# Kernel tuning notes

Hardware: AMD Instinct MI355X
Metric: run time of the kernel (lower is better)

The kernel has to match this reference:

```python
import jax, jax.numpy as jnp
import numpy as np

LN_EPS = 1e-5

def setup_inputs() -> dict:
    key = jax.random.key(0)
    k1, k2, k3 = jax.random.split(key, 3)
    L, B, D = 2048, 8, 1024
    x = jax.random.normal(k1, (L, B, D), dtype=jnp.float32)
    c = jnp.zeros((B, D), dtype=jnp.float32)
    W = jax.random.normal(k2, (D, 3 * D), dtype=jnp.float32) * 0.02
    # bias init from _init_bias: u-bias 0, f-bias 0.5, r-bias 0
    b = jnp.concatenate([jnp.zeros(D), jnp.full((D,), 0.5), jnp.zeros(D)]).astype(jnp.float32)
    gamma = jnp.ones((D,), dtype=jnp.float32)
    beta = jnp.zeros((D,), dtype=jnp.float32)
    return {"x": x, "c": c, "W": W, "b": b, "gamma": gamma, "beta": beta}

def reference(x, c, W, b, gamma, beta):
    # LayerNorm over last dim
    mu = jnp.mean(x, axis=-1, keepdims=True)
    var = jnp.mean(jnp.square(x - mu), axis=-1, keepdims=True)
    x_norm = (x - mu) * jax.lax.rsqrt(var + LN_EPS) * gamma + beta
    # Fused u/f/r projection: [L,B,3D]
    ufr = jnp.einsum('lbd,de->lbe', x_norm, W) + b
    u, f, r = jnp.split(ufr, 3, axis=-1)
    f_gate = jax.nn.sigmoid(f)
    r_gate = jax.nn.sigmoid(r)
    # Linear recurrence c_t = f_t * c_{t-1} + (1-f_t) * u_t via scan over time
    def step(c_prev, fu):
        f_t, u_t = fu
        c_t = f_t * c_prev + (1.0 - f_t) * u_t
        return c_t, c_t
    last_c, c_stack = jax.lax.scan(step, c, (f_gate, u))
    hs = r_gate * jnp.tanh(c_stack) + (1.0 - r_gate) * x_norm
    return x + hs, last_c
```

## Files before the change

### kernel.cpp

```cpp
#include <hip/hip_runtime.h>
#include <hip/hip_bf16.h>
#include <hip/hip_fp8.h>


typedef unsigned short u16;
typedef unsigned char u8;
typedef __bf16 bf16x8 __attribute__((ext_vector_type(8)));
typedef float f32x4 __attribute__((ext_vector_type(4)));
typedef long longx2 __attribute__((ext_vector_type(2)));

#define L_DIM 2048
#define B_DIM 8
#define D_DIM 1024
#define M_DIM (L_DIM * B_DIM)
#define K_DIM D_DIM
#define N_DIM (3 * D_DIM)
#define NCH 32
#define CLEN (L_DIM / NCH)
#define NT (K_DIM / 64)
#define NT8 (K_DIM / 128)

#define LDS_B 65536
#define LDS_DUMMY 131072
#define LDS_TOTAL 147456

__device__ __forceinline__ float bf2f(u16 h) {
    unsigned int u = ((unsigned int)h) << 16;
    float f;
    __builtin_memcpy(&f, &u, 4);
    return f;
}

__device__ __forceinline__ u16 f2bf(float f) {
    unsigned int u;
    __builtin_memcpy(&u, &f, 4);
    u = u + 0x7fff + ((u >> 16) & 1);
    return (u16)(u >> 16);
}

__device__ __forceinline__ u8 f2e4(float v) {
    __hip_fp8_e4m3 t(v);
    return (u8)t.__x;
}

__device__ __forceinline__ int kperm(int klocal) {
    int kk = klocal >> 5, lg = (klocal >> 3) & 3, e = klocal & 7;
    return (((kk >> 1) * 4 + lg) << 4) + ((kk & 1) << 3) + e;
}

__device__ __forceinline__ void async16(void* lds, const void* g) {
    __builtin_amdgcn_global_load_lds(
        (const __attribute__((address_space(1))) void*)g,
        (__attribute__((address_space(3))) void*)lds, 16, 0, 0);
}

__global__ __launch_bounds__(256) void ln_kernel(const float* __restrict__ x,
                                                 const float* __restrict__ gamma,
                                                 const float* __restrict__ beta,
                                                 u16* __restrict__ xn,
                                                 u8* __restrict__ xq,
                                                 float2* __restrict__ mrs) {
    int row = blockIdx.x;
    int tid = threadIdx.x;
    const float4* xr = (const float4*)(x + (size_t)row * D_DIM);
    float4 v = xr[tid];
    float s = v.x + v.y + v.z + v.w;
    float q = v.x * v.x + v.y * v.y + v.z * v.z + v.w * v.w;
    #pragma unroll
    for (int off = 32; off; off >>= 1) {
        s += __shfl_down(s, off);
        q += __shfl_down(q, off);
    }
    __shared__ float ss[4], qq[4];
    int lane = tid & 63, wv = tid >> 6;
    if (lane == 0) { ss[wv] = s; qq[wv] = q; }
    __syncthreads();
    s = ss[0] + ss[1] + ss[2] + ss[3];
    q = qq[0] + qq[1] + qq[2] + qq[3];
    float mu = s * (1.0f / D_DIM);
    float var = q * (1.0f / D_DIM) - mu * mu;
    float rs = rsqrtf(var + 1e-5f);
    if (tid == 0) mrs[row] = make_float2(mu, rs);
    float4 g = ((const float4*)gamma)[tid];
    float4 bt = ((const float4*)beta)[tid];
    float n0 = (v.x - mu) * rs * g.x + bt.x;
    float n1 = (v.y - mu) * rs * g.y + bt.y;
    float n2 = (v.z - mu) * rs * g.z + bt.z;
    float n3 = (v.w - mu) * rs * g.w + bt.w;
    ushort4 o;
    o.x = f2bf(n0); o.y = f2bf(n1); o.z = f2bf(n2); o.w = f2bf(n3);
    ((ushort4*)(xn + (size_t)row * D_DIM))[tid] = o;
    uchar4 o8;
    o8.x = f2e4(n0); o8.y = f2e4(n1); o8.z = f2e4(n2); o8.w = f2e4(n3);
    int k4 = tid * 4;
    int pos = (k4 & ~127) + kperm(k4 & 127);
    *(uchar4*)(xq + (size_t)row * D_DIM + pos) = o8;
}

__global__ __launch_bounds__(256) void wt_kernel(const float* __restrict__ W,
                                                 u16* __restrict__ Wt,
                                                 u8* __restrict__ Wf8) {
    __shared__ float t[64][65];
    int k0 = blockIdx.x * 64;
    int n0 = blockIdx.y * 64;
    int col = threadIdx.x & 63;
    int rg4 = threadIdx.x >> 6;
    #pragma unroll
    for (int j = 0; j < 16; ++j) {
        int r = rg4 * 16 + j;
        t[r][col] = W[(size_t)(k0 + r) * N_DIM + n0 + col];
    }
    __syncthreads();
    if (n0 < 1024) {
        #pragma unroll
        for (int j = 0; j < 16; ++j) {
            int nr = rg4 * 16 + j;
            Wt[(size_t)(n0 + nr) * K_DIM + k0 + col] = f2bf(t[col][nr]);
        }
    } else {
        #pragma unroll
        for (int j = 0; j < 16; ++j) {
            int nr = rg4 * 16 + j;
            int k = k0 + col;
            int pos = (k & ~127) + kperm(k & 127);
            Wf8[(size_t)(n0 - 1024 + nr) * K_DIM + pos] = f2e4(t[col][nr] * 64.0f);
        }
    }
}

__global__ __launch_bounds__(512, 2) void gemm_kernel(const u16* __restrict__ A,
                                                      const u16* __restrict__ Bt,
                                                      const float* __restrict__ bias,
                                                      u16* __restrict__ uo) {
    extern __shared__ char lds[];
    const int tid = threadIdx.x;
    const int wave = tid >> 6, lane = tid & 63;
    const int lm = lane & 15, lg = lane >> 4;
    const int wm = wave >> 2, wn = wave & 3;
    const int m0 = blockIdx.x * 256;
    const int n0 = blockIdx.y * 256;

    const int xk0 = ((0 | lg) ^ (lm & 7)) << 4;
    const int xk1 = ((4 | lg) ^ (lm & 7)) << 4;
    const char* pA0 = lds + (wm * 128 + lm) * 128 + xk0;
    const char* pA1 = lds + (wm * 128 + lm) * 128 + xk1;
    const char* pB0 = lds + LDS_B + (wn * 64 + lm) * 128 + xk0;
    const char* pB1 = lds + LDS_B + (wn * 64 + lm) * 128 + xk1;

    const int c1 = 512 + tid;
    const int r0 = tid >> 3, cc0 = (tid & 7) ^ (r0 & 7);
    const int r1 = c1 >> 3, cc1 = (c1 & 7) ^ (r1 & 7);
    const char* gA0 = (const char*)A + ((size_t)(m0 + r0) * K_DIM + cc0 * 8) * 2;
    const char* gA1 = (const char*)A + ((size_t)(m0 + r1) * K_DIM + cc1 * 8) * 2;
    const char* gB0 = (const char*)Bt + ((size_t)(n0 + r0) * K_DIM + cc0 * 8) * 2;
    const char* gB1 = (const char*)Bt + ((size_t)(n0 + r1) * K_DIM + cc1 * 8) * 2;
    char* dstW = lds + wave * 1024;

    f32x4 acc[8][4] = {};
    bf16x8 av[4], aw[4], bv0[4], bv1[4];

    auto stageA = [&](int t1, int h) {
        char* dst = (t1 < NT) ? (dstW + ((t1 & 1) << 15) + (h << 14))
                              : (lds + LDS_DUMMY + wave * 1024);
        int ko = ((t1 & 15) << 7) + (h << 18);
        async16(dst,        gA0 + ko);
        async16(dst + 8192, gA1 + ko);
    };
    auto stageB = [&](int t2, int h) {
        char* dst = (t2 < NT) ? (dstW + LDS_B + ((t2 & 1) << 15) + (h << 14))
                              : (lds + LDS_DUMMY + wave * 1024);
        int ko = ((t2 & 15) << 7) + (h << 18);
        async16(dst,        gB0 + ko);
        async16(dst + 8192, gB1 + ko);
    };

#define LDA(dst, pbase, bb, mf0)                                                \
    do { _Pragma("unroll")                                                      \
        for (int q = 0; q < 4; ++q)                                             \
            dst[q] = *(const bf16x8*)(pbase + (bb) * 32768 + ((mf0) + q) * 2048); \
    } while (0)

#define LDB(dst, pbase, bb)                                                     \
    do { _Pragma("unroll")                                                      \
        for (int nf = 0; nf < 4; ++nf)                                          \
            dst[nf] = *(const bf16x8*)(pbase + (bb) * 32768 + nf * 2048);       \
    } while (0)

#define MFMA16(r0q, afr, bfr)                                                   \
    do { _Pragma("unroll")                                                      \
        for (int q = 0; q < 4; ++q)                                             \
            _Pragma("unroll")                                                   \
            for (int nf = 0; nf < 4; ++nf)                                      \
                acc[(r0q) + q][nf] = __builtin_amdgcn_mfma_f32_16x16x32_bf16(   \
                    afr[q], bfr[nf], acc[(r0q) + q][nf], 0, 0, 0);              \
    } while (0)

#define PH_SYNC()                                                               \
    do { __builtin_amdgcn_s_barrier();                                          \
         asm volatile("s_waitcnt lgkmcnt(0)");                                  \
         __builtin_amdgcn_sched_barrier(0); } while (0)

#define TILE_BODY(t, bb)                                                        \
    do {                                                                        \
        LDA(av, pA0, bb, 0);                                                    \
        LDB(bv0, pB0, bb);                                                      \
        stageA((t) + 1, 0);                                                     \
        PH_SYNC();                                                              \
        __builtin_amdgcn_s_setprio(1);  MFMA16(0, av, bv0);                     \
        __builtin_amdgcn_s_setprio(0);  __builtin_amdgcn_s_barrier();           \
        LDA(av, pA1, bb, 0);                                                    \
        LDB(bv1, pB1, bb);                                                      \
        stageA((t) + 1, 1);                                                     \
        PH_SYNC();                                                              \
        __builtin_amdgcn_s_setprio(1);  MFMA16(0, av, bv1);                     \
        __builtin_amdgcn_s_setprio(0);  __builtin_amdgcn_s_barrier();           \
        LDA(aw, pA0, bb, 4);                                                    \
        stageB((t) + 2, 0);                                                     \
        PH_SYNC();                                                              \
        __builtin_amdgcn_s_setprio(1);  MFMA16(4, aw, bv0);                     \
        __builtin_amdgcn_s_setprio(0);  __builtin_amdgcn_s_barrier();           \
        LDA(aw, pA1, bb, 4);                                                    \
        stageB((t) + 2, 1);                                                     \
        PH_SYNC();                                                              \
        __builtin_amdgcn_s_setprio(1);  MFMA16(4, aw, bv1);                     \
        __builtin_amdgcn_s_setprio(0);                                          \
        asm volatile("s_waitcnt vmcnt(4)" ::: "memory");                        \
        __builtin_amdgcn_s_barrier();                                           \
    } while (0)

    stageA(0, 0); stageA(0, 1);
    stageB(0, 0); stageB(0, 1);
    stageB(1, 0); stageB(1, 1);
    asm volatile("s_waitcnt vmcnt(4)" ::: "memory");
    __builtin_amdgcn_s_barrier();

    for (int t = 0; t < NT; t += 2) {
        TILE_BODY(t, 0);
        TILE_BODY(t + 1, 1);
    }

    float bb4[4];
    #pragma unroll
    for (int nf = 0; nf < 4; ++nf) bb4[nf] = bias[n0 + wn * 64 + nf * 16 + lm];
    const int cmb = n0 + wn * 64 + lm;
    #pragma unroll
    for (int mf = 0; mf < 8; ++mf) {
        #pragma unroll
        for (int j = 0; j < 4; ++j) {
            int row = m0 + wm * 128 + mf * 16 + lg * 4 + j;
            u16* rp = uo + (size_t)row * D_DIM + cmb;
            #pragma unroll
            for (int nf = 0; nf < 4; ++nf)
                rp[nf * 16] = f2bf(acc[mf][nf][j] + bb4[nf]);
        }
    }
#undef LDA
#undef LDB
#undef MFMA16
#undef PH_SYNC
#undef TILE_BODY
}

__global__ __launch_bounds__(512, 2) void gemm8_kernel(const u8* __restrict__ A8,
                                                       const u8* __restrict__ B8,
                                                       const float* __restrict__ bias,
                                                       u16* __restrict__ fo,
                                                       u16* __restrict__ ro) {
    extern __shared__ char lds[];
    const int tid = threadIdx.x;
    const int wave = tid >> 6, lane = tid & 63;
    const int lm = lane & 15, lg = lane >> 4;
    const int wm = wave >> 2, wn = wave & 3;
    const int m0 = blockIdx.x * 256;
    const int n0 = blockIdx.y * 256;

    const int xj0 = (((0 * 4 + lg) ^ (lm & 7)) << 4);
    const int xj1 = (((1 * 4 + lg) ^ (lm & 7)) << 4);
    const char* pA = lds + (wm * 128 + lm) * 128;
    const char* pB = lds + LDS_B + (wn * 64 + lm) * 128;

    const int c1 = 512 + tid;
    const int r0 = tid >> 3, cc0 = (tid & 7) ^ (r0 & 7);
    const int r1 = c1 >> 3, cc1 = (c1 & 7) ^ (r1 & 7);
    const char* gA0 = (const char*)A8 + (size_t)(m0 + r0) * K_DIM + cc0 * 16;
    const char* gA1 = (const char*)A8 + (size_t)(m0 + r1) * K_DIM + cc1 * 16;
    const char* gB0 = (const char*)B8 + (size_t)(n0 + r0) * K_DIM + cc0 * 16;
    const char* gB1 = (const char*)B8 + (size_t)(n0 + r1) * K_DIM + cc1 * 16;
    char* dstW = lds + wave * 1024;

    f32x4 acc[8][4] = {};
    longx2 av[8], bv01[4], bv23[4];

    auto stageA = [&](int t1, int h) {
        char* dst = (t1 < NT8) ? (dstW + ((t1 & 1) << 15) + (h << 14))
                               : (lds + LDS_DUMMY + wave * 1024);
        int ko = ((t1 & 7) << 7) + (h << 17);
        async16(dst,        gA0 + ko);
        async16(dst + 8192, gA1 + ko);
    };
    auto stageB = [&](int t2, int h) {
        char* dst = (t2 < NT8) ? (dstW + LDS_B + ((t2 & 1) << 15) + (h << 14))
                               : (lds + LDS_DUMMY + wave * 1024);
        int ko = ((t2 & 7) << 7) + (h << 17);
        async16(dst,        gB0 + ko);
        async16(dst + 8192, gB1 + ko);
    };

#define LDA8(xj, bb)                                                            \
    do { _Pragma("unroll")                                                      \
        for (int q = 0; q < 8; ++q)                                             \
            av[q] = *(const longx2*)(pA + (bb) * 32768 + q * 2048 + (xj));      \
    } while (0)

#define LDB8(dst, xj, bb)                                                       \
    do { _Pragma("unroll")                                                      \
        for (int nf = 0; nf < 4; ++nf)                                          \
            dst[nf] = *(const longx2*)(pB + (bb) * 32768 + nf * 2048 + (xj));   \
    } while (0)

#define MFMA32F8(bfr, h)                                                        \
    do { _Pragma("unroll")                                                      \
        for (int q = 0; q < 8; ++q)                                             \
            _Pragma("unroll")                                                   \
            for (int nf = 0; nf < 4; ++nf)                                      \
                acc[q][nf] = __builtin_amdgcn_mfma_f32_16x16x32_fp8_fp8(        \
                    av[q][h], bfr[nf][h], acc[q][nf], 0, 0, 0);                 \
    } while (0)

#define PH_SYNC()                                                               \
    do { __builtin_amdgcn_s_barrier();                                          \
         asm volatile("s_waitcnt lgkmcnt(0)");                                  \
         __builtin_amdgcn_sched_barrier(0); } while (0)

#define TILE_BODY8(t, bb)                                                       \
    do {                                                                        \
        LDA8(xj0, bb);                                                          \
        LDB8(bv01, xj0, bb);                                                    \
        stageA((t) + 1, 0);                                                     \
        PH_SYNC();                                                              \
        __builtin_amdgcn_s_setprio(1);  MFMA32F8(bv01, 0);                      \
        __builtin_amdgcn_s_setprio(0);  __builtin_amdgcn_s_barrier();           \
        LDB8(bv23, xj1, bb);                                                    \
        stageA((t) + 1, 1);                                                     \
        PH_SYNC();                                                              \
        __builtin_amdgcn_s_setprio(1);  MFMA32F8(bv01, 1);                      \
        __builtin_amdgcn_s_setprio(0);  __builtin_amdgcn_s_barrier();           \
        LDA8(xj1, bb);                                                          \
        stageB((t) + 2, 0);                                                     \
        PH_SYNC();                                                              \
        __builtin_amdgcn_s_setprio(1);  MFMA32F8(bv23, 0);                      \
        __builtin_amdgcn_s_setprio(0);  __builtin_amdgcn_s_barrier();           \
        stageB((t) + 2, 1);                                                     \
        __builtin_amdgcn_s_barrier();                                           \
        __builtin_amdgcn_s_setprio(1);  MFMA32F8(bv23, 1);                      \
        __builtin_amdgcn_s_setprio(0);                                          \
        asm volatile("s_waitcnt vmcnt(4)" ::: "memory");                        \
        __builtin_amdgcn_s_barrier();                                           \
    } while (0)

    stageA(0, 0); stageA(0, 1);
    stageB(0, 0); stageB(0, 1);
    stageB(1, 0); stageB(1, 1);
    asm volatile("s_waitcnt vmcnt(4)" ::: "memory");
    __builtin_amdgcn_s_barrier();

    for (int t = 0; t < NT8; t += 2) {
        TILE_BODY8(t, 0);
        TILE_BODY8(t + 1, 1);
    }

    int seg = n0 >> 10;
    u16* outp = seg ? ro : fo;
    float bb4[4];
    #pragma unroll
    for (int nf = 0; nf < 4; ++nf) bb4[nf] = bias[1024 + n0 + wn * 64 + nf * 16 + lm];
    const int cmb = (n0 + wn * 64 + lm) & 1023;
    #pragma unroll
    for (int mf = 0; mf < 8; ++mf) {
        #pragma unroll
        for (int j = 0; j < 4; ++j) {
            int row = m0 + wm * 128 + mf * 16 + lg * 4 + j;
            u16* rp = outp + (size_t)row * D_DIM + cmb;
            #pragma unroll
            for (int nf = 0; nf < 4; ++nf) {
                float val = acc[mf][nf][j] * 0.015625f + bb4[nf];
                rp[nf * 16] = f2bf(1.0f / (1.0f + __expf(-val)));
            }
        }
    }
#undef LDA8
#undef LDB8
#undef MFMA32F8
#undef PH_SYNC
#undef TILE_BODY8
}

__global__ __launch_bounds__(256) void scan1_kernel(const u16* __restrict__ fg,
                                                    const u16* __restrict__ u,
                                                    float* __restrict__ Aa,
                                                    float* __restrict__ Ss) {
    int ch = blockIdx.x;
    int bd = (blockIdx.y * 256 + threadIdx.x) * 2;
    int b = bd >> 10, d = bd & 1023;
    float a0 = 1.0f, a1 = 1.0f, s0 = 0.0f, s1 = 0.0f;
    for (int t = ch * CLEN; t < ch * CLEN + CLEN; ++t) {
        size_t idx = ((size_t)(t * B_DIM + b) << 10) + d;
        ushort2 f2 = *(const ushort2*)(fg + idx);
        ushort2 u2 = *(const ushort2*)(u + idx);
        float f0 = bf2f(f2.x), f1 = bf2f(f2.y);
        float v0 = bf2f(u2.x), v1 = bf2f(u2.y);
        s0 = f0 * s0 + (1.0f - f0) * v0;
        s1 = f1 * s1 + (1.0f - f1) * v1;
        a0 *= f0;
        a1 *= f1;
    }
    int o = ch * 8192 + bd;
    *(float2*)(Aa + o) = make_float2(a0, a1);
    *(float2*)(Ss + o) = make_float2(s0, s1);
}

__global__ __launch_bounds__(256) void scan2_kernel(const float* __restrict__ Aa,
                                                    const float* __restrict__ Ss,
                                                    const float* __restrict__ c0,
                                                    float* __restrict__ cs,
                                                    float* __restrict__ lastc) {
    int bd = blockIdx.x * 256 + threadIdx.x;
    float c = c0[bd];
    #pragma unroll 4
    for (int ch = 0; ch < NCH; ++ch) {
        cs[ch * 8192 + bd] = c;
        c = Aa[ch * 8192 + bd] * c + Ss[ch * 8192 + bd];
    }
    lastc[bd] = c;
}

__global__ __launch_bounds__(256) void scan3_kernel(const float* __restrict__ cs,
                                                    const u16* __restrict__ fg,
                                                    const u16* __restrict__ u,
                                                    const u16* __restrict__ rg,
                                                    const float2* __restrict__ mrs,
                                                    const float* __restrict__ gamma,
                                                    const float* __restrict__ beta,
                                                    const float* __restrict__ x,
                                                    float* __restrict__ out) {
    int ch = blockIdx.x;
    int bd = (blockIdx.y * 256 + threadIdx.x) * 2;
    int b = bd >> 10, d = bd & 1023;
    float2 gm = *(const float2*)(gamma + d);
    float2 bt = *(const float2*)(beta + d);
    float c0v = cs[ch * 8192 + bd];
    float c1v = cs[ch * 8192 + bd + 1];
    for (int t = ch * CLEN; t < ch * CLEN + CLEN; ++t) {
        size_t idx = ((size_t)(t * B_DIM + b) << 10) + d;
        ushort2 f2 = *(const ushort2*)(fg + idx);
        ushort2 u2 = *(const ushort2*)(u + idx);
        ushort2 r2 = *(const ushort2*)(rg + idx);
        float2 x2 = *(const float2*)(x + idx);
        float2 mr = mrs[t * B_DIM + b];
        float f0 = bf2f(f2.x), f1 = bf2f(f2.y);
        float v0 = bf2f(u2.x), v1 = bf2f(u2.y);
        float r0 = bf2f(r2.x), r1 = bf2f(r2.y);
        float n0 = (x2.x - mr.x) * mr.y * gm.x + bt.x;
        float n1 = (x2.y - mr.x) * mr.y * gm.y + bt.y;
        c0v = f0 * c0v + (1.0f - f0) * v0;
        c1v = f1 * c1v + (1.0f - f1) * v1;
        float h0 = r0 * tanhf(c0v) + (1.0f - r0) * n0;
        float h1 = r1 * tanhf(c1v) + (1.0f - r1) * n1;
        *(float2*)(out + idx) = make_float2(x2.x + h0, x2.y + h1);
    }
}

extern "C" void kernel_launch(void* const* d_in, const int* in_sizes, int n_in,
                              void* d_out, int out_size, void* d_ws, size_t ws_size,
                              hipStream_t stream) {
    const float* x     = (const float*)d_in[0];
    const float* c0    = (const float*)d_in[1];
    const float* W     = (const float*)d_in[2];
    const float* b     = (const float*)d_in[3];
    const float* gamma = (const float*)d_in[4];
    const float* beta  = (const float*)d_in[5];
    float* out = (float*)d_out;
    float* lastc = out + (size_t)M_DIM * D_DIM;
    u8* xq = (u8*)d_out;

    char* w = (char*)d_ws;
    u16* xn = (u16*)w;  w += (size_t)M_DIM * D_DIM * 2;
    u16* Wt = (u16*)w;  w += (size_t)N_DIM * K_DIM * 2;
    u16* ug = (u16*)w;  w += (size_t)M_DIM * D_DIM * 2;
    u16* fg = (u16*)w;  w += (size_t)M_DIM * D_DIM * 2;
    u16* rg = (u16*)w;  w += (size_t)M_DIM * D_DIM * 2;
    float* Aa = (float*)w; w += (size_t)NCH * 8192 * 4;
    float* Ss = (float*)w; w += (size_t)NCH * 8192 * 4;
    float* cs = (float*)w; w += (size_t)NCH * 8192 * 4;
    float2* mrs = (float2*)w; w += (size_t)M_DIM * 8;
    u8* Wf8 = (u8*)w; w += (size_t)2048 * K_DIM;

    hipFuncSetAttribute(reinterpret_cast<const void*>(gemm_kernel),
                        hipFuncAttributeMaxDynamicSharedMemorySize, LDS_TOTAL);
    hipFuncSetAttribute(reinterpret_cast<const void*>(gemm8_kernel),
                        hipFuncAttributeMaxDynamicSharedMemorySize, LDS_TOTAL);

    ln_kernel<<<M_DIM, 256, 0, stream>>>(x, gamma, beta, xn, xq, mrs);
    wt_kernel<<<dim3(K_DIM / 64, N_DIM / 64), 256, 0, stream>>>(W, Wt, Wf8);
    gemm_kernel<<<dim3(M_DIM / 256, 4), 512, LDS_TOTAL, stream>>>(xn, Wt, b, ug);
    gemm8_kernel<<<dim3(M_DIM / 256, 8), 512, LDS_TOTAL, stream>>>(xq, Wf8, b, fg, rg);
    scan1_kernel<<<dim3(NCH, 16), 256, 0, stream>>>(fg, ug, Aa, Ss);
    scan2_kernel<<<32, 256, 0, stream>>>(Aa, Ss, c0, cs, lastc);
    scan3_kernel<<<dim3(NCH, 16), 256, 0, stream>>>(cs, fg, ug, rg, mrs, gamma, beta, x, out);
}
```

Measured before the change: 196.8 us.

## Halve FP8 GEMM N-tile, single-buffer B in LDS, raise occupancy target

```diff
diff --git a/kernel.cpp b/kernel.cpp
--- a/kernel.cpp
+++ b/kernel.cpp
@@ -23,6 +23,8 @@
 #define LDS_B 65536
 #define LDS_DUMMY 131072
 #define LDS_TOTAL 147456
+#define L8_B 65536
+#define L8_TOTAL 81920
 
 __device__ __forceinline__ float bf2f(u16 h) {
     unsigned int u = ((unsigned int)h) << 16;
@@ -261,7 +263,7 @@
 #undef TILE_BODY
 }
 
-__global__ __launch_bounds__(512, 2) void gemm8_kernel(const u8* __restrict__ A8,
+__global__ __launch_bounds__(512, 4) void gemm8_kernel(const u8* __restrict__ A8,
                                                        const u8* __restrict__ B8,
                                                        const float* __restrict__ bias,
                                                        u16* __restrict__ fo,
@@ -272,12 +274,12 @@
     const int lm = lane & 15, lg = lane >> 4;
     const int wm = wave >> 2, wn = wave & 3;
     const int m0 = blockIdx.x * 256;
-    const int n0 = blockIdx.y * 256;
-
-    const int xj0 = (((0 * 4 + lg) ^ (lm & 7)) << 4);
-    const int xj1 = (((1 * 4 + lg) ^ (lm & 7)) << 4);
+    const int n0 = blockIdx.y * 128;
+
+    const int xj0 = ((lg ^ (lm & 7)) << 4);
+    const int xj1 = (((4 + lg) ^ (lm & 7)) << 4);
     const char* pA = lds + (wm * 128 + lm) * 128;
-    const char* pB = lds + LDS_B + (wn * 64 + lm) * 128;
+    const char* pB = lds + L8_B + (wn * 32 + lm) * 128;
 
     const int c1 = 512 + tid;
     const int r0 = tid >> 3, cc0 = (tid & 7) ^ (r0 & 7);
@@ -288,20 +290,20 @@
     const char* gB1 = (const char*)B8 + (size_t)(n0 + r1) * K_DIM + cc1 * 16;
     char* dstW = lds + wave * 1024;
 
-    f32x4 acc[8][4] = {};
-    longx2 av[8], bv01[4], bv23[4];
+    f32x4 acc[8][2] = {};
+    longx2 av[8], bv01[2], bv23[2];
 
     auto stageA = [&](int t1, int h) {
-        char* dst = (t1 < NT8) ? (dstW + ((t1 & 1) << 15) + (h << 14))
-                               : (lds + LDS_DUMMY + wave * 1024);
+        if (t1 >= NT8) return;
+        char* dst = dstW + ((t1 & 1) << 15) + (h << 14);
         int ko = ((t1 & 7) << 7) + (h << 17);
         async16(dst,        gA0 + ko);
         async16(dst + 8192, gA1 + ko);
     };
-    auto stageB = [&](int t2, int h) {
-        char* dst = (t2 < NT8) ? (dstW + LDS_B + ((t2 & 1) << 15) + (h << 14))
-                               : (lds + LDS_DUMMY + wave * 1024);
-        int ko = ((t2 & 7) << 7) + (h << 17);
+    auto stageB = [&](int t1) {
+        if (t1 >= NT8) return;
+        char* dst = dstW + L8_B;
+        int ko = (t1 & 7) << 7;
         async16(dst,        gB0 + ko);
         async16(dst + 8192, gB1 + ko);
     };
@@ -312,17 +314,17 @@
             av[q] = *(const longx2*)(pA + (bb) * 32768 + q * 2048 + (xj));      \
     } while (0)
 
-#define LDB8(dst, xj, bb)                                                       \
+#define LDB8(dst, xj)                                                           \
     do { _Pragma("unroll")                                                      \
-        for (int nf = 0; nf < 4; ++nf)                                          \
-            dst[nf] = *(const longx2*)(pB + (bb) * 32768 + nf * 2048 + (xj));   \
-    } while (0)
-
-#define MFMA32F8(bfr, h)                                                        \
+        for (int nf = 0; nf < 2; ++nf)                                          \
+            dst[nf] = *(const longx2*)(pB + nf * 2048 + (xj));                  \
+    } while (0)
+
+#define MFMA16F8(bfr, h)                                                        \
     do { _Pragma("unroll")                                                      \
         for (int q = 0; q < 8; ++q)                                             \
             _Pragma("unroll")                                                   \
-            for (int nf = 0; nf < 4; ++nf)                                      \
+            for (int nf = 0; nf < 2; ++nf)                                      \
                 acc[q][nf] = __builtin_amdgcn_mfma_f32_16x16x32_fp8_fp8(        \
                     av[q][h], bfr[nf][h], acc[q][nf], 0, 0, 0);                 \
     } while (0)
@@ -334,36 +336,37 @@
 
 #define TILE_BODY8(t, bb)                                                       \
     do {                                                                        \
+                                                                   \
         LDA8(xj0, bb);                                                          \
-        LDB8(bv01, xj0, bb);                                                    \
+        LDB8(bv01, xj0);                                                        \
         stageA((t) + 1, 0);                                                     \
         PH_SYNC();                                                              \
-        __builtin_amdgcn_s_setprio(1);  MFMA32F8(bv01, 0);                      \
+        __builtin_amdgcn_s_setprio(1);  MFMA16F8(bv01, 0);                      \
         __builtin_amdgcn_s_setprio(0);  __builtin_amdgcn_s_barrier();           \
-        LDB8(bv23, xj1, bb);                                                    \
+                                                                   \
+        LDB8(bv23, xj1);                                                        \
         stageA((t) + 1, 1);                                                     \
         PH_SYNC();                                                              \
-        __builtin_amdgcn_s_setprio(1);  MFMA32F8(bv01, 1);                      \
+        __builtin_amdgcn_s_setprio(1);  MFMA16F8(bv01, 1);                      \
         __builtin_amdgcn_s_setprio(0);  __builtin_amdgcn_s_barrier();           \
+                          \
         LDA8(xj1, bb);                                                          \
-        stageB((t) + 2, 0);                                                     \
-        PH_SYNC();                                                              \
-        __builtin_amdgcn_s_setprio(1);  MFMA32F8(bv23, 0);                      \
+        stageB((t) + 1);                                                        \
+        PH_SYNC();                                                              \
+        __builtin_amdgcn_s_setprio(1);  MFMA16F8(bv23, 0);                      \
         __builtin_amdgcn_s_setprio(0);  __builtin_amdgcn_s_barrier();           \
-        stageB((t) + 2, 1);                                                     \
+                                                         \
+        __builtin_amdgcn_s_setprio(1);  MFMA16F8(bv23, 1);                      \
+        __builtin_amdgcn_s_setprio(0);                                          \
+        asm volatile("s_waitcnt vmcnt(0)" ::: "memory");                        \
         __builtin_amdgcn_s_barrier();                                           \
-        __builtin_amdgcn_s_setprio(1);  MFMA32F8(bv23, 1);                      \
-        __builtin_amdgcn_s_setprio(0);                                          \
-        asm volatile("s_waitcnt vmcnt(4)" ::: "memory");                        \
-        __builtin_amdgcn_s_barrier();                                           \
-    } while (0)
-
-    stageA(0, 0); stageA(0, 1);
-    stageB(0, 0); stageB(0, 1);
-    stageB(1, 0); stageB(1, 1);
-    asm volatile("s_waitcnt vmcnt(4)" ::: "memory");
+    } while (0)
+
+    stageA(0, 0); stageA(0, 1); stageB(0);
+    asm volatile("s_waitcnt vmcnt(0)" ::: "memory");
     __builtin_amdgcn_s_barrier();
 
+    #pragma unroll 1
     for (int t = 0; t < NT8; t += 2) {
         TILE_BODY8(t, 0);
         TILE_BODY8(t + 1, 1);
@@ -371,10 +374,10 @@
 
     int seg = n0 >> 10;
     u16* outp = seg ? ro : fo;
-    float bb4[4];
+    float bb2[2];
     #pragma unroll
-    for (int nf = 0; nf < 4; ++nf) bb4[nf] = bias[1024 + n0 + wn * 64 + nf * 16 + lm];
-    const int cmb = (n0 + wn * 64 + lm) & 1023;
+    for (int nf = 0; nf < 2; ++nf) bb2[nf] = bias[1024 + n0 + wn * 32 + nf * 16 + lm];
+    const int cmb = (n0 & 1023) + wn * 32 + lm;
     #pragma unroll
     for (int mf = 0; mf < 8; ++mf) {
         #pragma unroll
@@ -382,15 +385,15 @@
             int row = m0 + wm * 128 + mf * 16 + lg * 4 + j;
             u16* rp = outp + (size_t)row * D_DIM + cmb;
             #pragma unroll
-            for (int nf = 0; nf < 4; ++nf) {
-                float val = acc[mf][nf][j] * 0.015625f + bb4[nf];
+            for (int nf = 0; nf < 2; ++nf) {
+                float val = acc[mf][nf][j] * 0.015625f + bb2[nf];
                 rp[nf * 16] = f2bf(1.0f / (1.0f + __expf(-val)));
             }
         }
     }
 #undef LDA8
 #undef LDB8
-#undef MFMA32F8
+#undef MFMA16F8
 #undef PH_SYNC
 #undef TILE_BODY8
 }
@@ -498,12 +501,12 @@
     hipFuncSetAttribute(reinterpret_cast<const void*>(gemm_kernel),
                         hipFuncAttributeMaxDynamicSharedMemorySize, LDS_TOTAL);
     hipFuncSetAttribute(reinterpret_cast<const void*>(gemm8_kernel),
-                        hipFuncAttributeMaxDynamicSharedMemorySize, LDS_TOTAL);
+                        hipFuncAttributeMaxDynamicSharedMemorySize, L8_TOTAL);
 
     ln_kernel<<<M_DIM, 256, 0, stream>>>(x, gamma, beta, xn, xq, mrs);
     wt_kernel<<<dim3(K_DIM / 64, N_DIM / 64), 256, 0, stream>>>(W, Wt, Wf8);
     gemm_kernel<<<dim3(M_DIM / 256, 4), 512, LDS_TOTAL, stream>>>(xn, Wt, b, ug);
-    gemm8_kernel<<<dim3(M_DIM / 256, 8), 512, LDS_TOTAL, stream>>>(xq, Wf8, b, fg, rg);
+    gemm8_kernel<<<dim3(M_DIM / 256, 16), 512, L8_TOTAL, stream>>>(xq, Wf8, b, fg, rg);
     scan1_kernel<<<dim3(NCH, 16), 256, 0, stream>>>(fg, ug, Aa, Ss);
     scan2_kernel<<<32, 256, 0, stream>>>(Aa, Ss, c0, cs, lastc);
     scan3_kernel<<<dim3(NCH, 16), 256, 0, stream>>>(cs, fg, ug, rg, mrs, gamma, beta, x, out);
```

After: 228.4 us. +16.0%, slower.
